# Optimization experiments

Measured on AMD Instinct MI355X. Metric: run time of the kernel, lower is better.

## Reference

```python
import jax, jax.numpy as jnp
import numpy as np

B, S, H, DH = 1, 4096, 8, 40  # hardcoded in the original forward
D = H * DH  # 320

def setup_inputs() -> dict:
    key = jax.random.key(0)
    ks = jax.random.split(key, 6)
    s = 1.0 / np.sqrt(D)
    return {
        "x": jax.random.normal(ks[0], (B, S, D), dtype=jnp.float32),
        "Wq": jax.random.normal(ks[1], (D, D), dtype=jnp.float32) * s,
        "Wk": jax.random.normal(ks[2], (D, D), dtype=jnp.float32) * s,
        "Wv": jax.random.normal(ks[3], (D, D), dtype=jnp.float32) * s,
        "Wo": jax.random.normal(ks[4], (D, D), dtype=jnp.float32) * s,
        "bo": jnp.zeros((D,), dtype=jnp.float32),
    }

def reference(x, Wq, Wk, Wv, Wo, bo):
    scale = DH ** (-0.5)
    # nn.Linear(bias=False): y = x @ W^T. context = x (self-attention).
    q = x @ Wq.T
    k = x @ Wk.T
    v = x @ Wv.T
    # split heads: [B,S,D] -> [B*H, S, DH]
    def split_heads(t):
        return t.reshape(B, S, H, DH).transpose(0, 2, 1, 3).reshape(B * H, S, DH)
    q, k, v = split_heads(q), split_heads(k), split_heads(v)
    # fp32 QK^T (original forces float), softmax, AV
    sim = jnp.einsum('bid,bjd->bij', q.astype(jnp.float32), k.astype(jnp.float32)) * scale
    attn = jax.nn.softmax(sim, axis=-1)
    out = jnp.einsum('bij,bjd->bid', attn, v)
    # merge heads: [B*H, S, DH] -> [B, S, D]
    out = out.reshape(B, H, S, DH).transpose(0, 2, 1, 3).reshape(B, S, D)
    return out @ Wo.T + bo
```

## Files before the change

kernel.cpp:

```cpp
#include <hip/hip_runtime.h>
#include <math.h>


#define NS 4096
#define ND 320
#define SCALE2 0.2281101152f
#define HS48 196608
#define VTH 163840
#define XN 1310720

typedef __attribute__((ext_vector_type(8))) short bf16x8;
typedef __attribute__((ext_vector_type(16))) float f32x16;

static __device__ __forceinline__ unsigned short f2b(float f) {
  unsigned int u = __builtin_bit_cast(unsigned int, f);
  u += 0x7fffu + ((u >> 16) & 1u);
  return (unsigned short)(u >> 16);
}
static __device__ __forceinline__ unsigned int pk2rne(float a, float b) {
  return (unsigned int)f2b(a) | ((unsigned int)f2b(b) << 16);
}
static __device__ __forceinline__ unsigned int pk2t(float a, float b) {
  return __builtin_amdgcn_perm(__builtin_bit_cast(unsigned int, b),
                               __builtin_bit_cast(unsigned int, a), 0x07060302u);
}
static __device__ __forceinline__ float fexp2(float x) {
  return __builtin_amdgcn_exp2f(x);
}
static __device__ __forceinline__ bf16x8 ld8(const unsigned short* p) {
  union { uint2 u[2]; bf16x8 v; } c;
  c.u[0] = *(const uint2*)p;
  c.u[1] = *(const uint2*)(p + 4);
  return c.v;
}
static __device__ __forceinline__ void st16(unsigned short* p, uint4 v) {
  *(uint2*)p = make_uint2(v.x, v.y);
  *(uint2*)(p + 4) = make_uint2(v.z, v.w);
}
static __device__ __forceinline__ int sig32(int q) {
  int s = q >> 4, h2 = (q >> 3) & 1, j = q & 7;
  return (s << 4) | ((j >> 2) << 3) | (h2 << 2) | (j & 3);
}

__global__ __launch_bounds__(256) void proj_qkv_kernel(
    const float* __restrict__ x, const float* __restrict__ Wq,
    const float* __restrict__ Wk, const float* __restrict__ Wv,
    unsigned short* __restrict__ Qp, unsigned short* __restrict__ Kp,
    unsigned short* __restrict__ Vt) {
  const int z = blockIdx.z;
  const float* W = (z == 0) ? Wq : (z == 1) ? Wk : Wv;
  __shared__ __align__(16) unsigned short As[64 * 36];
  __shared__ __align__(16) unsigned short Bs[64 * 36];
  const int t = threadIdx.x;
  const int w = t >> 6, l = t & 63, l31 = l & 31, hi = l >> 5;
  const int bm = blockIdx.x * 64, bn = blockIdx.y * 64;
  const int m0 = (w & 1) * 32, n0 = (w >> 1) * 32;
  f32x16 acc = {0,0,0,0,0,0,0,0,0,0,0,0,0,0,0,0};
  const int ar = t >> 2, ac = t & 3;
  const float* gA = x + (bm + ar) * ND + ac * 8;
  const float* gB = W + (bn + ar) * ND + ac * 8;
  unsigned short* lA = As + ar * 36 + ac * 8;
  unsigned short* lB = Bs + ar * 36 + ac * 8;
  const unsigned short* af = As + (m0 + l31) * 36 + hi * 8;
  const unsigned short* bf = Bs + (n0 + l31) * 36 + hi * 8;
  float4 a0 = *(const float4*)gA, a1 = *(const float4*)(gA + 4);
  float4 b0 = *(const float4*)gB, b1 = *(const float4*)(gB + 4);
  for (int k0 = 0; k0 < ND; k0 += 32) {
    __syncthreads();
    st16(lA, make_uint4(pk2rne(a0.x, a0.y), pk2rne(a0.z, a0.w),
                        pk2rne(a1.x, a1.y), pk2rne(a1.z, a1.w)));
    st16(lB, make_uint4(pk2rne(b0.x, b0.y), pk2rne(b0.z, b0.w),
                        pk2rne(b1.x, b1.y), pk2rne(b1.z, b1.w)));
    __syncthreads();
    if (k0 + 32 < ND) {
      gA += 32; gB += 32;
      a0 = *(const float4*)gA; a1 = *(const float4*)(gA + 4);
      b0 = *(const float4*)gB; b1 = *(const float4*)(gB + 4);
    }
    bf16x8 A0 = ld8(af), A1 = ld8(af + 16);
    bf16x8 B0 = ld8(bf), B1 = ld8(bf + 16);
    acc = __builtin_amdgcn_mfma_f32_32x32x16_bf16(A0, B0, acc, 0, 0, 0);
    acc = __builtin_amdgcn_mfma_f32_32x32x16_bf16(A1, B1, acc, 0, 0, 0);
  }
  const int j = bn + n0 + l31;
  const int h = j / 40, dh = j - h * 40;
  if (z < 2) {
    unsigned short* Y = (z == 0) ? Qp : Kp;
    const float sc = (z == 0) ? SCALE2 : 1.0f;
    const unsigned short padv = (z == 0) ? (unsigned short)0xC200u
                                         : (unsigned short)0x3F80u;
#pragma unroll
    for (int r = 0; r < 16; r++) {
      int row = bm + m0 + (r & 3) + 8 * (r >> 2) + 4 * hi;
      Y[h * HS48 + row * 48 + dh] = f2b(acc[r] * sc);
      if (dh < 8)
        Y[h * HS48 + row * 48 + 40 + dh] = (dh == 0) ? padv : (unsigned short)0;
    }
  } else {
#pragma unroll
    for (int r = 0; r < 16; r++) {
      int row = bm + m0 + (r & 3) + 8 * (r >> 2) + 4 * hi;
      Vt[h * VTH + dh * NS + row] = f2b(acc[r]);
    }
  }
}

__global__ __launch_bounds__(256) void attn_kernel(
    const unsigned short* __restrict__ Qp, const unsigned short* __restrict__ Kp,
    const unsigned short* __restrict__ Vt, unsigned short* __restrict__ Op,
    float* __restrict__ Lp) {
  const int b = blockIdx.x;
  const int h = b & 7, ks = (b >> 3) & 7, qt = b >> 6;
  const int t = threadIdx.x;
  const int w = t >> 6, l = t & 63, l31 = l & 31, hi = l >> 5;
  __shared__ __align__(16) unsigned short Ks[64 * 68];
  __shared__ __align__(16) unsigned short Vs[48 * 68];
  for (int i = t; i < 272; i += 256)
    ((unsigned int*)(Vs + 40 * 68))[i] = (i < 34) ? 0x3F803F80u : 0u;

  const int kbase = ks * 512;
  const int qbase = qt * 128 + w * 32;
  const unsigned short* qp = Qp + h * HS48 + (qbase + l31) * 48 + hi * 8;
  bf16x8 qf0 = *(const bf16x8*)qp;
  bf16x8 qf1 = *(const bf16x8*)(qp + 16);
  bf16x8 qf2 = *(const bf16x8*)(qp + 32);

  f32x16 oa0 = {0,0,0,0,0,0,0,0,0,0,0,0,0,0,0,0};
  f32x16 oa1 = {0,0,0,0,0,0,0,0,0,0,0,0,0,0,0,0};

  const int kr0 = t / 6, kc0 = t - kr0 * 6;
  const int kr1 = (t + 256) / 6, kc1 = (t + 256) - kr1 * 6;
  const unsigned short* gK0 = Kp + h * HS48 + (kbase + kr0) * 48 + kc0 * 8;
  const unsigned short* gK1 = Kp + h * HS48 + (kbase + kr1) * 48 + kc1 * 8;
  unsigned short* lK0 = Ks + ((kr0 & 32) | sig32(kr0 & 31)) * 68 + kc0 * 8;
  unsigned short* lK1 = Ks + ((kr1 & 32) | sig32(kr1 & 31)) * 68 + kc1 * 8;
  const int vr0 = t >> 3, vc = t & 7, vr1 = 32 + vr0;
  const unsigned short* gV0 = Vt + h * VTH + vr0 * NS + kbase + vc * 8;
  const unsigned short* gV1 = Vt + h * VTH + vr1 * NS + kbase + vc * 8;
  unsigned short* lV0 = Vs + vr0 * 68 + vc * 8;
  unsigned short* lV1 = Vs + vr1 * 68 + vc * 8;

  const unsigned short* kf0 = Ks + l31 * 68 + hi * 8;
  const unsigned short* kf1 = Ks + (32 + l31) * 68 + hi * 8;
  const unsigned short* vf0 = Vs + l31 * 68 + hi * 8;
  const unsigned short* vf1 = Vs + (32 + (l31 & 15)) * 68 + hi * 8;

  uint4 ka = *(const uint4*)gK0;
  uint4 kb2, vb2;
  uint4 va = *(const uint4*)gV0;
  if (t < 128) kb2 = *(const uint4*)gK1;
  if (t < 64)  vb2 = *(const uint4*)gV1;

  for (int it = 0; it < 8; ++it) {
    __syncthreads();
    st16(lK0, ka);
    if (t < 128) st16(lK1, kb2);
    st16(lV0, va);
    if (t < 64) st16(lV1, vb2);
    __syncthreads();
    gK0 += 64 * 48; gK1 += 64 * 48; gV0 += 64; gV1 += 64;
    ka = *(const uint4*)gK0;
    va = *(const uint4*)gV0;
    if (t < 128) kb2 = *(const uint4*)gK1;
    if (t < 64)  vb2 = *(const uint4*)gV1;

    unsigned int pw0[8], pw1[8];
    {
      f32x16 s0 = {0,0,0,0,0,0,0,0,0,0,0,0,0,0,0,0};
      s0 = __builtin_amdgcn_mfma_f32_32x32x16_bf16(ld8(kf0), qf0, s0, 0, 0, 0);
      s0 = __builtin_amdgcn_mfma_f32_32x32x16_bf16(ld8(kf0 + 16), qf1, s0, 0, 0, 0);
      s0 = __builtin_amdgcn_mfma_f32_32x32x16_bf16(ld8(kf0 + 32), qf2, s0, 0, 0, 0);
#pragma unroll
      for (int i = 0; i < 8; i++)
        pw0[i] = pk2t(fexp2(s0[2 * i]), fexp2(s0[2 * i + 1]));
    }
    {
      f32x16 s1 = {0,0,0,0,0,0,0,0,0,0,0,0,0,0,0,0};
      s1 = __builtin_amdgcn_mfma_f32_32x32x16_bf16(ld8(kf1), qf0, s1, 0, 0, 0);
      s1 = __builtin_amdgcn_mfma_f32_32x32x16_bf16(ld8(kf1 + 16), qf1, s1, 0, 0, 0);
      s1 = __builtin_amdgcn_mfma_f32_32x32x16_bf16(ld8(kf1 + 32), qf2, s1, 0, 0, 0);
#pragma unroll
      for (int i = 0; i < 8; i++)
        pw1[i] = pk2t(fexp2(s1[2 * i]), fexp2(s1[2 * i + 1]));
    }
    bf16x8 pf0 = __builtin_bit_cast(bf16x8, make_uint4(pw0[0], pw0[1], pw0[2], pw0[3]));
    bf16x8 pf1 = __builtin_bit_cast(bf16x8, make_uint4(pw0[4], pw0[5], pw0[6], pw0[7]));
    bf16x8 pf2 = __builtin_bit_cast(bf16x8, make_uint4(pw1[0], pw1[1], pw1[2], pw1[3]));
    bf16x8 pf3 = __builtin_bit_cast(bf16x8, make_uint4(pw1[4], pw1[5], pw1[6], pw1[7]));
    oa0 = __builtin_amdgcn_mfma_f32_32x32x16_bf16(pf0, ld8(vf0), oa0, 0, 0, 0);
    oa1 = __builtin_amdgcn_mfma_f32_32x32x16_bf16(pf0, ld8(vf1), oa1, 0, 0, 0);
    oa0 = __builtin_amdgcn_mfma_f32_32x32x16_bf16(pf1, ld8(vf0 + 16), oa0, 0, 0, 0);
    oa1 = __builtin_amdgcn_mfma_f32_32x32x16_bf16(pf1, ld8(vf1 + 16), oa1, 0, 0, 0);
    oa0 = __builtin_amdgcn_mfma_f32_32x32x16_bf16(pf2, ld8(vf0 + 32), oa0, 0, 0, 0);
    oa1 = __builtin_amdgcn_mfma_f32_32x32x16_bf16(pf2, ld8(vf1 + 32), oa1, 0, 0, 0);
    oa0 = __builtin_amdgcn_mfma_f32_32x32x16_bf16(pf3, ld8(vf0 + 48), oa0, 0, 0, 0);
    oa1 = __builtin_amdgcn_mfma_f32_32x32x16_bf16(pf3, ld8(vf1 + 48), oa1, 0, 0, 0);
  }

  unsigned short* opb = Op + ks * 1310720 + h * 163840;
  float* lpb = Lp + ks * 32768 + h * NS;
#pragma unroll
  for (int r = 0; r < 16; r++) {
    int qr = qbase + (r & 3) + 8 * (r >> 2) + 4 * hi;
    opb[qr * 40 + l31] = f2b(oa0[r]);
    if (l31 < 8) opb[qr * 40 + 32 + l31] = f2b(oa1[r]);
    if (l31 == 8) lpb[qr] = oa1[r];
  }
}

__global__ __launch_bounds__(256) void combine_kernel(
    const unsigned short* __restrict__ Op, const float* __restrict__ Lp,
    unsigned short* __restrict__ Xo) {
  int e = (blockIdx.x * 256 + threadIdx.x) * 2;
  int h = e / 163840;
  int r = e - h * 163840;
  int s = r / 40;
  int dh = r - s * 40;
  float a0 = 0.f, a1 = 0.f, lsum = 0.f;
#pragma unroll
  for (int k = 0; k < 8; k++) {
    unsigned int u = *(const unsigned int*)(Op + k * 1310720 + e);
    a0 += __builtin_bit_cast(float, u << 16);
    a1 += __builtin_bit_cast(float, u & 0xFFFF0000u);
    lsum += Lp[k * 32768 + h * NS + s];
  }
  float inv = 1.0f / lsum;
  *(unsigned int*)(Xo + s * ND + h * 40 + dh) = pk2rne(a0 * inv, a1 * inv);
}

__global__ __launch_bounds__(256) void proj_out_kernel(
    const unsigned short* __restrict__ Xo, const float* __restrict__ Wo,
    const float* __restrict__ bo, float* __restrict__ out) {
  __shared__ __align__(16) unsigned short As[64 * 36];
  __shared__ __align__(16) unsigned short Bs[64 * 36];
  const int t = threadIdx.x;
  const int w = t >> 6, l = t & 63, l31 = l & 31, hi = l >> 5;
  const int bm = blockIdx.x * 64, bn = blockIdx.y * 64;
  const int m0 = (w & 1) * 32, n0 = (w >> 1) * 32;
  f32x16 acc = {0,0,0,0,0,0,0,0,0,0,0,0,0,0,0,0};
  const int ar = t >> 2, ac = t & 3;
  const unsigned short* gA = Xo + (bm + ar) * ND + ac * 8;
  const float* gB = Wo + (bn + ar) * ND + ac * 8;
  unsigned short* lA = As + ar * 36 + ac * 8;
  unsigned short* lB = Bs + ar * 36 + ac * 8;
  const unsigned short* af = As + (m0 + l31) * 36 + hi * 8;
  const unsigned short* bf = Bs + (n0 + l31) * 36 + hi * 8;
  uint4 a = *(const uint4*)gA;
  float4 b0 = *(const float4*)gB, b1 = *(const float4*)(gB + 4);
  for (int k0 = 0; k0 < ND; k0 += 32) {
    __syncthreads();
    st16(lA, a);
    st16(lB, make_uint4(pk2rne(b0.x, b0.y), pk2rne(b0.z, b0.w),
                        pk2rne(b1.x, b1.y), pk2rne(b1.z, b1.w)));
    __syncthreads();
    if (k0 + 32 < ND) {
      gA += 32; gB += 32;
      a = *(const uint4*)gA;
      b0 = *(const float4*)gB; b1 = *(const float4*)(gB + 4);
    }
    bf16x8 A0 = ld8(af), A1 = ld8(af + 16);
    bf16x8 B0 = ld8(bf), B1 = ld8(bf + 16);
    acc = __builtin_amdgcn_mfma_f32_32x32x16_bf16(A0, B0, acc, 0, 0, 0);
    acc = __builtin_amdgcn_mfma_f32_32x32x16_bf16(A1, B1, acc, 0, 0, 0);
  }
  const int j = bn + n0 + l31;
  const float bj = bo[j];
#pragma unroll
  for (int r = 0; r < 16; r++) {
    int row = bm + m0 + (r & 3) + 8 * (r >> 2) + 4 * hi;
    out[row * ND + j] = acc[r] + bj;
  }
}

extern "C" void kernel_launch(void* const* d_in, const int* in_sizes, int n_in,
                              void* d_out, int out_size, void* d_ws, size_t ws_size,
                              hipStream_t stream) {
  (void)in_sizes; (void)n_in; (void)out_size; (void)ws_size;
  const float* x  = (const float*)d_in[0];
  const float* Wq = (const float*)d_in[1];
  const float* Wk = (const float*)d_in[2];
  const float* Wv = (const float*)d_in[3];
  const float* Wo = (const float*)d_in[4];
  const float* bo = (const float*)d_in[5];
  float* out = (float*)d_out;

  unsigned short* Qp = (unsigned short*)d_ws;
  unsigned short* Kp = Qp + 8 * HS48;
  unsigned short* Vt = Kp + 8 * HS48;
  unsigned short* Xo = Vt + 8 * VTH;
  unsigned short* Op = Xo + XN;
  float* Lp = (float*)(Op + 8 * XN);

  proj_qkv_kernel<<<dim3(64, 5, 3), 256, 0, stream>>>(x, Wq, Wk, Wv, Qp, Kp, Vt);
  attn_kernel<<<dim3(2048), 256, 0, stream>>>(Qp, Kp, Vt, Op, Lp);
  combine_kernel<<<dim3(2560), 256, 0, stream>>>(Op, Lp, Xo);
  proj_out_kernel<<<dim3(64, 5), 256, 0, stream>>>(Xo, Wo, bo, out);
}
```

Before: 132.8 us.

## Fuse split-K combine into output projection and stage QKV stores through LDS

Removes the separate combine kernel. The output projection now sums the eight split-K partial outputs and normalises them by the summed denominators while loading its A tiles, so the Xo intermediate and one launch are gone. The QKV projection stages its results in an LDS tile, including a transpose for V, and then writes them to global memory as 16-byte vectors instead of scattered 2-byte stores. Float-to-bf16 conversion changes from round-to-nearest-even to a cheaper round-half-up. The trade-off is that each of the five output-projection column blocks re-reads the same partials, so that traffic is repeated five times.

```diff
diff --git a/kernel.cpp b/kernel.cpp
--- a/kernel.cpp
+++ b/kernel.cpp
@@ -12,13 +12,13 @@
 typedef __attribute__((ext_vector_type(8))) short bf16x8;
 typedef __attribute__((ext_vector_type(16))) float f32x16;
 
-static __device__ __forceinline__ unsigned short f2b(float f) {
-  unsigned int u = __builtin_bit_cast(unsigned int, f);
-  u += 0x7fffu + ((u >> 16) & 1u);
-  return (unsigned short)(u >> 16);
-}
-static __device__ __forceinline__ unsigned int pk2rne(float a, float b) {
-  return (unsigned int)f2b(a) | ((unsigned int)f2b(b) << 16);
+static __device__ __forceinline__ unsigned short f2bru(float f) {
+  return (unsigned short)((__builtin_bit_cast(unsigned int, f) + 0x8000u) >> 16);
+}
+static __device__ __forceinline__ unsigned int pk2ru(float a, float b) {
+  unsigned int ua = __builtin_bit_cast(unsigned int, a) + 0x8000u;
+  unsigned int ub = __builtin_bit_cast(unsigned int, b) + 0x8000u;
+  return __builtin_amdgcn_perm(ub, ua, 0x07060302u);
 }
 static __device__ __forceinline__ unsigned int pk2t(float a, float b) {
   return __builtin_amdgcn_perm(__builtin_bit_cast(unsigned int, b),
@@ -32,6 +32,10 @@
   c.u[0] = *(const uint2*)p;
   c.u[1] = *(const uint2*)(p + 4);
   return c.v;
+}
+static __device__ __forceinline__ uint4 ld16u(const unsigned short* p) {
+  uint2 a = *(const uint2*)p, b = *(const uint2*)(p + 4);
+  return make_uint4(a.x, a.y, b.x, b.y);
 }
 static __device__ __forceinline__ void st16(unsigned short* p, uint4 v) {
   *(uint2*)p = make_uint2(v.x, v.y);
@@ -51,6 +55,7 @@
   const float* W = (z == 0) ? Wq : (z == 1) ? Wk : Wv;
   __shared__ __align__(16) unsigned short As[64 * 36];
   __shared__ __align__(16) unsigned short Bs[64 * 36];
+  __shared__ __align__(16) unsigned short Tile[64 * 76];
   const int t = threadIdx.x;
   const int w = t >> 6, l = t & 63, l31 = l & 31, hi = l >> 5;
   const int bm = blockIdx.x * 64, bn = blockIdx.y * 64;
@@ -67,10 +72,10 @@
   float4 b0 = *(const float4*)gB, b1 = *(const float4*)(gB + 4);
   for (int k0 = 0; k0 < ND; k0 += 32) {
     __syncthreads();
-    st16(lA, make_uint4(pk2rne(a0.x, a0.y), pk2rne(a0.z, a0.w),
-                        pk2rne(a1.x, a1.y), pk2rne(a1.z, a1.w)));
-    st16(lB, make_uint4(pk2rne(b0.x, b0.y), pk2rne(b0.z, b0.w),
-                        pk2rne(b1.x, b1.y), pk2rne(b1.z, b1.w)));
+    st16(lA, make_uint4(pk2ru(a0.x, a0.y), pk2ru(a0.z, a0.w),
+                        pk2ru(a1.x, a1.y), pk2ru(a1.z, a1.w)));
+    st16(lB, make_uint4(pk2ru(b0.x, b0.y), pk2ru(b0.z, b0.w),
+                        pk2ru(b1.x, b1.y), pk2ru(b1.z, b1.w)));
     __syncthreads();
     if (k0 + 32 < ND) {
       gA += 32; gB += 32;
@@ -82,25 +87,39 @@
     acc = __builtin_amdgcn_mfma_f32_32x32x16_bf16(A0, B0, acc, 0, 0, 0);
     acc = __builtin_amdgcn_mfma_f32_32x32x16_bf16(A1, B1, acc, 0, 0, 0);
   }
-  const int j = bn + n0 + l31;
-  const int h = j / 40, dh = j - h * 40;
   if (z < 2) {
     unsigned short* Y = (z == 0) ? Qp : Kp;
     const float sc = (z == 0) ? SCALE2 : 1.0f;
-    const unsigned short padv = (z == 0) ? (unsigned short)0xC200u
-                                         : (unsigned short)0x3F80u;
-#pragma unroll
-    for (int r = 0; r < 16; r++) {
-      int row = bm + m0 + (r & 3) + 8 * (r >> 2) + 4 * hi;
-      Y[h * HS48 + row * 48 + dh] = f2b(acc[r] * sc);
-      if (dh < 8)
-        Y[h * HS48 + row * 48 + 40 + dh] = (dh == 0) ? padv : (unsigned short)0;
+    const unsigned int padw = (z == 0) ? 0xC200u : 0x3F80u;
+#pragma unroll
+    for (int r2 = 0; r2 < 16; r2++) {
+      int lr = m0 + (r2 & 3) + 8 * (r2 >> 2) + 4 * hi;
+      Tile[lr * 68 + n0 + l31] = f2bru(acc[r2] * sc);
+    }
+    __syncthreads();
+    for (int i = t; i < 512; i += 256) {
+      int row = i >> 3, ch = i & 7;
+      int j = bn + ch * 8;
+      int h = j / 40, dh = j - h * 40;
+      uint4 v = ld16u(Tile + row * 68 + ch * 8);
+      unsigned short* dst = Y + h * HS48 + (bm + row) * 48 + dh;
+      st16(dst, v);
+      if (dh == 0)
+        st16(Y + h * HS48 + (bm + row) * 48 + 40, make_uint4(padw, 0u, 0u, 0u));
     }
   } else {
 #pragma unroll
-    for (int r = 0; r < 16; r++) {
-      int row = bm + m0 + (r & 3) + 8 * (r >> 2) + 4 * hi;
-      Vt[h * VTH + dh * NS + row] = f2b(acc[r]);
+    for (int r2 = 0; r2 < 16; r2++) {
+      int lr = m0 + (r2 & 3) + 8 * (r2 >> 2) + 4 * hi;
+      Tile[(n0 + l31) * 76 + lr] = f2bru(acc[r2]);
+    }
+    __syncthreads();
+    for (int i = t; i < 512; i += 256) {
+      int row = i >> 3, ch = i & 7;
+      int j = bn + row;
+      int h = j / 40, dd = j - h * 40;
+      uint4 v = ld16u(Tile + row * 76 + ch * 8);
+      st16(Vt + h * VTH + dd * NS + bm + ch * 8, v);
     }
   }
 }
@@ -197,65 +216,83 @@
     oa1 = __builtin_amdgcn_mfma_f32_32x32x16_bf16(pf3, ld8(vf1 + 48), oa1, 0, 0, 0);
   }
 
-  unsigned short* opb = Op + ks * 1310720 + h * 163840;
+  unsigned short* opb = Op + ks * XN + h * 163840;
   float* lpb = Lp + ks * 32768 + h * NS;
 #pragma unroll
-  for (int r = 0; r < 16; r++) {
-    int qr = qbase + (r & 3) + 8 * (r >> 2) + 4 * hi;
-    opb[qr * 40 + l31] = f2b(oa0[r]);
-    if (l31 < 8) opb[qr * 40 + 32 + l31] = f2b(oa1[r]);
-    if (l31 == 8) lpb[qr] = oa1[r];
-  }
-}
-
-__global__ __launch_bounds__(256) void combine_kernel(
+  for (int r2 = 0; r2 < 16; r2++) {
+    int qr = qbase + (r2 & 3) + 8 * (r2 >> 2) + 4 * hi;
+    opb[qr * 40 + l31] = f2bru(oa0[r2]);
+    if (l31 < 8) opb[qr * 40 + 32 + l31] = f2bru(oa1[r2]);
+    if (l31 == 8) lpb[qr] = oa1[r2];
+  }
+}
+
+__global__ __launch_bounds__(256) void proj_out_kernel(
     const unsigned short* __restrict__ Op, const float* __restrict__ Lp,
-    unsigned short* __restrict__ Xo) {
-  int e = (blockIdx.x * 256 + threadIdx.x) * 2;
-  int h = e / 163840;
-  int r = e - h * 163840;
-  int s = r / 40;
-  int dh = r - s * 40;
-  float a0 = 0.f, a1 = 0.f, lsum = 0.f;
-#pragma unroll
-  for (int k = 0; k < 8; k++) {
-    unsigned int u = *(const unsigned int*)(Op + k * 1310720 + e);
-    a0 += __builtin_bit_cast(float, u << 16);
-    a1 += __builtin_bit_cast(float, u & 0xFFFF0000u);
-    lsum += Lp[k * 32768 + h * NS + s];
-  }
-  float inv = 1.0f / lsum;
-  *(unsigned int*)(Xo + s * ND + h * 40 + dh) = pk2rne(a0 * inv, a1 * inv);
-}
-
-__global__ __launch_bounds__(256) void proj_out_kernel(
-    const unsigned short* __restrict__ Xo, const float* __restrict__ Wo,
-    const float* __restrict__ bo, float* __restrict__ out) {
+    const float* __restrict__ Wo, const float* __restrict__ bo,
+    float* __restrict__ out) {
   __shared__ __align__(16) unsigned short As[64 * 36];
   __shared__ __align__(16) unsigned short Bs[64 * 36];
+  __shared__ float invL[512];
   const int t = threadIdx.x;
   const int w = t >> 6, l = t & 63, l31 = l & 31, hi = l >> 5;
   const int bm = blockIdx.x * 64, bn = blockIdx.y * 64;
   const int m0 = (w & 1) * 32, n0 = (w >> 1) * 32;
   f32x16 acc = {0,0,0,0,0,0,0,0,0,0,0,0,0,0,0,0};
   const int ar = t >> 2, ac = t & 3;
-  const unsigned short* gA = Xo + (bm + ar) * ND + ac * 8;
+
+  for (int i = t; i < 512; i += 256) {
+    int h2 = i >> 6, sl = i & 63;
+    float ls = 0.f;
+#pragma unroll
+    for (int k = 0; k < 8; k++) ls += Lp[k * 32768 + h2 * NS + bm + sl];
+    invL[i] = 1.0f / ls;
+  }
+
   const float* gB = Wo + (bn + ar) * ND + ac * 8;
   unsigned short* lA = As + ar * 36 + ac * 8;
   unsigned short* lB = Bs + ar * 36 + ac * 8;
   const unsigned short* af = As + (m0 + l31) * 36 + hi * 8;
   const unsigned short* bf = Bs + (n0 + l31) * 36 + hi * 8;
-  uint4 a = *(const uint4*)gA;
+
+  int d0 = ac * 8;
+  int h2 = d0 / 40, dh = d0 - h2 * 40;
+  const unsigned short* opb = Op + h2 * 163840 + (bm + ar) * 40 + dh;
+  uint4 u[8];
+#pragma unroll
+  for (int k = 0; k < 8; k++) u[k] = *(const uint4*)(opb + k * XN);
   float4 b0 = *(const float4*)gB, b1 = *(const float4*)(gB + 4);
+
   for (int k0 = 0; k0 < ND; k0 += 32) {
     __syncthreads();
-    st16(lA, a);
-    st16(lB, make_uint4(pk2rne(b0.x, b0.y), pk2rne(b0.z, b0.w),
-                        pk2rne(b1.x, b1.y), pk2rne(b1.z, b1.w)));
+    {
+      float a0 = 0.f, a1 = 0.f, a2 = 0.f, a3 = 0.f;
+      float a4 = 0.f, a5 = 0.f, a6 = 0.f, a7 = 0.f;
+#pragma unroll
+      for (int k = 0; k < 8; k++) {
+        a0 += __builtin_bit_cast(float, u[k].x << 16);
+        a1 += __builtin_bit_cast(float, u[k].x & 0xFFFF0000u);
+        a2 += __builtin_bit_cast(float, u[k].y << 16);
+        a3 += __builtin_bit_cast(float, u[k].y & 0xFFFF0000u);
+        a4 += __builtin_bit_cast(float, u[k].z << 16);
+        a5 += __builtin_bit_cast(float, u[k].z & 0xFFFF0000u);
+        a6 += __builtin_bit_cast(float, u[k].w << 16);
+        a7 += __builtin_bit_cast(float, u[k].w & 0xFFFF0000u);
+      }
+      float inv = invL[h2 * 64 + ar];
+      st16(lA, make_uint4(pk2ru(a0 * inv, a1 * inv), pk2ru(a2 * inv, a3 * inv),
+                          pk2ru(a4 * inv, a5 * inv), pk2ru(a6 * inv, a7 * inv)));
+    }
+    st16(lB, make_uint4(pk2ru(b0.x, b0.y), pk2ru(b0.z, b0.w),
+                        pk2ru(b1.x, b1.y), pk2ru(b1.z, b1.w)));
     __syncthreads();
     if (k0 + 32 < ND) {
-      gA += 32; gB += 32;
-      a = *(const uint4*)gA;
+      d0 += 32;
+      h2 = d0 / 40; dh = d0 - h2 * 40;
+      opb = Op + h2 * 163840 + (bm + ar) * 40 + dh;
+#pragma unroll
+      for (int k = 0; k < 8; k++) u[k] = *(const uint4*)(opb + k * XN);
+      gB += 32;
       b0 = *(const float4*)gB; b1 = *(const float4*)(gB + 4);
     }
     bf16x8 A0 = ld8(af), A1 = ld8(af + 16);
@@ -266,9 +303,9 @@
   const int j = bn + n0 + l31;
   const float bj = bo[j];
 #pragma unroll
-  for (int r = 0; r < 16; r++) {
-    int row = bm + m0 + (r & 3) + 8 * (r >> 2) + 4 * hi;
-    out[row * ND + j] = acc[r] + bj;
+  for (int r2 = 0; r2 < 16; r2++) {
+    int row = bm + m0 + (r2 & 3) + 8 * (r2 >> 2) + 4 * hi;
+    out[row * ND + j] = acc[r2] + bj;
   }
 }
 
@@ -287,12 +324,10 @@
   unsigned short* Qp = (unsigned short*)d_ws;
   unsigned short* Kp = Qp + 8 * HS48;
   unsigned short* Vt = Kp + 8 * HS48;
-  unsigned short* Xo = Vt + 8 * VTH;
-  unsigned short* Op = Xo + XN;
+  unsigned short* Op = Vt + 8 * VTH;
   float* Lp = (float*)(Op + 8 * XN);
 
   proj_qkv_kernel<<<dim3(64, 5, 3), 256, 0, stream>>>(x, Wq, Wk, Wv, Qp, Kp, Vt);
   attn_kernel<<<dim3(2048), 256, 0, stream>>>(Qp, Kp, Vt, Op, Lp);
-  combine_kernel<<<dim3(2560), 256, 0, stream>>>(Op, Lp, Xo);
-  proj_out_kernel<<<dim3(64, 5), 256, 0, stream>>>(Xo, Wo, bo, out);
-}
+  proj_out_kernel<<<dim3(64, 5), 256, 0, stream>>>(Op, Lp, Wo, bo, out);
+}
```

Measured after the change: 135.4 us. About the same (+1.9%).
